# Kernel optimization log

Measured on AMD Instinct MI355X. Metric: run time of the kernel, lower is better.

## Reference

```python
import jax, jax.numpy as jnp
import numpy as np

PAD = 7                 # init padding
T = 2 * PAD + 1         # T_side_dense = 15 shifts per axis
LAMDA = 1.0             # init lamda
EPS = 1e-16             # hardcoded epsilon in the torch loss body


def _joint_hist(x_out, x_tf_out):
    # Equivalent of F.conv2d(x_out.permute(1,0,2,3), weight=x_tf_out.permute(1,0,2,3), padding=PAD)
    # expressed as T*T shifted matmuls (correlation / cost-volume form).
    bn, k, h, w = x_out.shape
    A = jnp.transpose(x_out, (1, 0, 2, 3))      # (k, bn, h, w)  conv "input"
    B = jnp.transpose(x_tf_out, (1, 0, 2, 3))   # (k, bn, h, w)  conv "weight"
    A_pad = jnp.pad(A, ((0, 0), (0, 0), (PAD, PAD), (PAD, PAD)))

    def step(carry, s):
        dy, dx = s // T, s % T
        sl = jax.lax.dynamic_slice(A_pad, (0, 0, dy, dx), (k, bn, h, w))
        # p[n, o] at this shift = sum_{c,y,x} A_pad[n,c,y+dy,x+dx] * B[o,c,y,x]
        return carry, jnp.einsum('nchw,ochw->no', sl, B)

    _, p = jax.lax.scan(step, None, jnp.arange(T * T))
    # (T*T, k, k) -> (T, T, k, k); matches torch p_i_j.permute(2, 3, 0, 1)
    return p.reshape(T, T, k, k)


def reference(x_out, x_tf_out):
    p = _joint_hist(x_out, x_tf_out)
    # shift to positive; min is detached in torch -> stop_gradient
    p = p - jax.lax.stop_gradient(p.min()) + EPS
    # normalize per shift over the (k, k) joint
    p = p / p.sum(axis=(2, 3), keepdims=True)
    # symmetrize
    p = (p + jnp.swapaxes(p, 2, 3)) / 2.0
    p_i = p.sum(axis=2, keepdims=True)   # (T, T, 1, k) marginal (broadcasts like repeat)
    p_j = p.sum(axis=3, keepdims=True)   # (T, T, k, 1) marginal
    loss = (-p * (jnp.log(p + EPS)
                  - LAMDA * jnp.log(p_i + EPS)
                  - LAMDA * jnp.log(p_j + EPS))).sum() / (T * T)
    return loss


def setup_inputs() -> dict:
    key = jax.random.key(0)
    k1, k2 = jax.random.split(key)
    bn, k, h, w = 16, 10, 224, 224
    # simplex over axis=1 is asserted by the torch module -> use softmax
    x_out = jax.nn.softmax(jax.random.normal(k1, (bn, k, h, w), dtype=jnp.float32), axis=1)
    x_tf_out = jax.nn.softmax(jax.random.normal(k2, (bn, k, h, w), dtype=jnp.float32), axis=1)
    return {"x_out": x_out, "x_tf_out": x_tf_out}
```

## Files before the change

### kernel.cpp

```cpp
#include <hip/hip_runtime.h>
#include <stdint.h>
#include <math.h>


#define PADV 7
#define TS 15
#define KCLS 10
#define HH 224
#define WW 224
#define MD 160
#define NCELL (MD*MD)
#define NBLK 256
#define TY 14
#define BSTRIDE 232
#define BSTRIDE_L 236
#define BPH 240
#define PLANEE 2408
#define ABUFE (8*PLANEE)
#define NRED 400
#define LEPS 1e-16

typedef __attribute__((ext_vector_type(4))) float f32x4;
typedef __attribute__((ext_vector_type(8))) short bf16x8;

__device__ __forceinline__ unsigned short f2bf(float f) {
  union { float f; uint32_t u; } v; v.f = f;
  return (unsigned short)((v.u + 0x7FFFu + ((v.u >> 16) & 1u)) >> 16);
}

__device__ __forceinline__ uint32_t pack2bf(float a, float b) {
  return (uint32_t)f2bf(a) | ((uint32_t)f2bf(b) << 16);
}

__device__ __forceinline__ void glds16(const unsigned short* g, unsigned short* l) {
  __builtin_amdgcn_global_load_lds(
      (const __attribute__((address_space(1))) unsigned int*)g,
      (__attribute__((address_space(3))) unsigned int*)l, 16, 0, 0);
}

__device__ __forceinline__ void plane_write(const f32x4 f[4], unsigned short* awr) {
  uint32_t w[8];
#pragma unroll
  for (int k = 0; k < 8; ++k)
    w[k] = pack2bf(f[k >> 1][(k & 1) * 2], f[k >> 1][(k & 1) * 2 + 1]);
#pragma unroll
  for (int c = 0; c < 8; ++c) {
    union { uint32_t u[4]; uint4 v; } o;
    if (c & 1) {
#pragma unroll
      for (int j = 0; j < 4; ++j) o.u[j] = w[j + (c + 1) / 2];
    } else {
#pragma unroll
      for (int j = 0; j < 4; ++j)
        o.u[j] = __builtin_amdgcn_alignbit(w[j + 1 + c / 2], w[j + c / 2], 16);
    }
    *(uint4*)(awr + c * PLANEE) = o.v;
  }
}

__global__ __launch_bounds__(256)
void prep_b(const float* __restrict__ xt, unsigned short* __restrict__ bp) {
  const int idx   = blockIdx.x * 256 + threadIdx.x;
  const int rowid = idx / 29;
  const int chunk = idx - rowid * 29;
  const int x0    = chunk * 8;
  const int yy    = rowid % BPH;
  const int cls   = rowid / BPH;
  const int row   = yy - PADV;
  union { unsigned short h[8]; uint4 v; } out;
  if (row >= 0 && row < HH && chunk < 28) {
    const float4* src = (const float4*)(xt + ((size_t)cls * HH + row) * WW + x0);
    const float4 f0 = src[0], f1 = src[1];
    out.h[0] = f2bf(f0.x); out.h[1] = f2bf(f0.y);
    out.h[2] = f2bf(f0.z); out.h[3] = f2bf(f0.w);
    out.h[4] = f2bf(f1.x); out.h[5] = f2bf(f1.y);
    out.h[6] = f2bf(f1.z); out.h[7] = f2bf(f1.w);
  } else {
    out.v = make_uint4(0u, 0u, 0u, 0u);
  }
  *(uint4*)(bp + (size_t)rowid * BSTRIDE + x0) = out.v;
}

#define MFMA_BF16 __builtin_amdgcn_mfma_f32_16x16x32_bf16

__global__ __launch_bounds__(640, 1)
void corr_gemm(const float* __restrict__ xo, const unsigned short* __restrict__ bpad,
               float* __restrict__ partials) {
  __shared__ __align__(16) unsigned short ldsA8[2 * ABUFE];
  __shared__ __align__(16) unsigned short ldsB[KCLS * 16 * BSTRIDE_L];

  const int tid  = threadIdx.x;
  const int bid0 = blockIdx.x;
  const int bid  = (bid0 & 7) * 32 + (bid0 >> 3);
  const int b    = bid >> 4;
  const int y0   = (bid & 15) * TY;

  const int lane = tid & 63;
  const int wv   = tid >> 6;
  const int wm   = wv >> 1;
  const int wn   = wv & 1;
  const int quad = lane >> 4;
  const int l15  = lane & 15;

  f32x4 acc[2][5];
#pragma unroll
  for (int i = 0; i < 2; ++i)
#pragma unroll
    for (int j = 0; j < 5; ++j) acc[i][j] = (f32x4){0.f, 0.f, 0.f, 0.f};

  const float* Ab = xo + (size_t)b * KCLS * HH * WW;
  const unsigned short* Bb = bpad + (size_t)b * KCLS * BPH * BSTRIDE;

  const bool aw  = tid < 300;
  const int an   = aw ? tid / 30 : 0;
  const int atp  = aw ? tid - (tid / 30) * 30 : 0;
  const int axb  = atp * 8 - 8;
  bool gv[4];
#pragma unroll
  for (int g = 0; g < 4; ++g)
    gv[g] = aw && (axb + 4 * g >= 0) && (axb + 4 * g + 4 <= WW);
  unsigned short* const awr0 = ldsA8 + an * 240 + atp * 8;

  for (int pr = wv; pr < 15 * KCLS; pr += 10) {
    const int r15  = pr / KCLS;
    const int o    = pr - r15 * KCLS;
    const int yy   = y0 + r15;
    const int slot = (y0 - PADV + r15) & 15;
    if (lane < 29)
      glds16(Bb + ((size_t)o * BPH + yy) * BSTRIDE + lane * 8,
             ldsB + (o * 16 + slot) * BSTRIDE_L);
  }

  f32x4 f[4];
  {
    const float* src = Ab + ((size_t)an * HH + y0) * WW + axb;
#pragma unroll
    for (int g = 0; g < 4; ++g) {
      f[g] = (f32x4){0.f, 0.f, 0.f, 0.f};
      if (gv[g]) f[g] = *(const f32x4*)(src + 4 * g);
    }
  }
  if (aw) plane_write(f, awr0);
  __syncthreads();

  int cur = 0;
  for (int s = 0; s < TY; ++s) {
    const int y = y0 + s;
    const bool more = (s + 1 < TY);

    if (more) {
      const int yy   = y + 8 + PADV;
      const int slot = (y + 8) & 15;
      if (lane < 29)
        glds16(Bb + ((size_t)wv * BPH + yy) * BSTRIDE + lane * 8,
               ldsB + (wv * 16 + slot) * BSTRIDE_L);
      const float* src = Ab + ((size_t)an * HH + (y + 1)) * WW + axb;
#pragma unroll
      for (int g = 0; g < 4; ++g) {
        f[g] = (f32x4){0.f, 0.f, 0.f, 0.f};
        if (gv[g]) f[g] = *(const f32x4*)(src + 4 * g);
      }
    }

    const unsigned short* paB = ldsA8 + cur * ABUFE + (l15 & 7) * PLANEE + (l15 & 8);
    const int slotB = (y + PADV - l15) & 15;

#pragma unroll 2
    for (int xc = 0; xc < 7; ++xc) {
      const int x0 = xc * 32;
      bf16x8 afrag[2], bfrag[5];
#pragma unroll
      for (int mi = 0; mi < 2; ++mi)
        afrag[mi] = *(const bf16x8*)(paB + (wm * 2 + mi) * 240 + x0 + quad * 8);
#pragma unroll
      for (int ni = 0; ni < 5; ++ni) {
        const int to = wn * 5 + ni;
        bfrag[ni] = *(const bf16x8*)(ldsB + (to * 16 + slotB) * BSTRIDE_L + x0 + quad * 8);
      }
#pragma unroll
      for (int mi = 0; mi < 2; ++mi)
#pragma unroll
        for (int ni = 0; ni < 5; ++ni)
          acc[mi][ni] = MFMA_BF16(afrag[mi], bfrag[ni], acc[mi][ni], 0, 0, 0);
    }

    if (more) {
      if (aw) plane_write(f, awr0 + (cur ^ 1) * ABUFE);
      __syncthreads();
      cur ^= 1;
    }
  }

  float* outp = partials + (size_t)bid * NCELL;
#pragma unroll
  for (int mi = 0; mi < 2; ++mi)
#pragma unroll
    for (int ni = 0; ni < 5; ++ni) {
      const int mrow = (wm * 2 + mi) * 16 + quad * 4;
      const int ncol = (wn * 5 + ni) * 16 + l15;
#pragma unroll
      for (int r = 0; r < 4; ++r)
        outp[(size_t)(mrow + r) * MD + ncol] = acc[mi][ni][r];
    }
}

__global__ __launch_bounds__(256)
void reduce_all(const float* __restrict__ partials, float* __restrict__ Cout,
                float* __restrict__ mins, float* __restrict__ dout) {
  const int tid = threadIdx.x;
  const int cl  = tid & 63;
  const int g   = tid >> 6;
  const int c   = blockIdx.x * 64 + cl;
  if (blockIdx.x == 0 && tid == 0) dout[0] = 0.f;

  const float* base = partials + (size_t)g * 64 * NCELL + c;
  double s0 = 0.0, s1 = 0.0, s2 = 0.0, s3 = 0.0;
  for (int p = 0; p < 64; p += 4) {
    s0 += (double)base[(size_t)(p + 0) * NCELL];
    s1 += (double)base[(size_t)(p + 1) * NCELL];
    s2 += (double)base[(size_t)(p + 2) * NCELL];
    s3 += (double)base[(size_t)(p + 3) * NCELL];
  }
  __shared__ double redd[256];
  redd[tid] = (s0 + s1) + (s2 + s3);
  __syncthreads();

  __shared__ float redm[64];
  if (tid < 64) {
    const double tot = redd[tid] + redd[tid + 64] + redd[tid + 128] + redd[tid + 192];
    const float sf = (float)tot;
    Cout[c] = sf;
    const int m  = c / MD;
    const int nn = c - m * MD;
    const bool valid = ((m & 15) < TS) && ((nn & 15) < TS);
    redm[tid] = valid ? sf : 3.4e38f;
  }
  __syncthreads();
  for (int st = 32; st > 0; st >>= 1) {
    if (tid < st) redm[tid] = fminf(redm[tid], redm[tid + st]);
    __syncthreads();
  }
  if (tid == 0) mins[blockIdx.x] = redm[0];
}

__global__ __launch_bounds__(128)
void loss_kernel(const float* __restrict__ Cmat, const float* __restrict__ mins,
                 float* __restrict__ dout) {
  const int s   = blockIdx.x;
  const int dy  = s / TS;
  const int dx  = s - dy * TS;
  const int tid = threadIdx.x;
  __shared__ float fm[128];
  __shared__ double q[100];
  __shared__ double sym[100];
  __shared__ double pi[10], pj[10];
  __shared__ double red[128];

  {
    float v = 3.4e38f;
    for (int i = tid; i < NRED; i += 128) v = fminf(v, mins[i]);
    fm[tid] = v;
  }
  __syncthreads();
  for (int st = 64; st > 0; st >>= 1) {
    if (tid < st) fm[tid] = fminf(fm[tid], fm[tid + st]);
    __syncthreads();
  }
  const double minv = (double)fm[0];
  __syncthreads();

  if (tid < 100) {
    const int n = tid / 10, o = tid - (tid / 10) * 10;
    const double v = (double)Cmat[(size_t)(n * 16 + dx) * MD + (o * 16 + dy)];
    q[tid] = v - minv + LEPS;
  }
  __syncthreads();
  red[tid] = (tid < 100) ? q[tid] : 0.0;
  __syncthreads();
  for (int st = 64; st > 0; st >>= 1) {
    if (tid < st) red[tid] += red[tid + st];
    __syncthreads();
  }
  const double Z = red[0];
  __syncthreads();
  if (tid < 100) {
    const int n = tid / 10, o = tid - (tid / 10) * 10;
    sym[tid] = (q[n * 10 + o] + q[o * 10 + n]) * 0.5 / Z;
  }
  __syncthreads();
  if (tid < 10) {
    double a = 0.0, bsum = 0.0;
    for (int n2 = 0; n2 < 10; ++n2) {
      a    += sym[n2 * 10 + tid];
      bsum += sym[tid * 10 + n2];
    }
    pi[tid] = a;
    pj[tid] = bsum;
  }
  __syncthreads();
  double term = 0.0;
  if (tid < 100) {
    const int n = tid / 10, o = tid - (tid / 10) * 10;
    const double sp = sym[tid];
    term = -sp * (log(sp + LEPS) - log(pi[o] + LEPS) - log(pj[n] + LEPS));
  }
  red[tid] = term;
  __syncthreads();
  for (int st = 64; st > 0; st >>= 1) {
    if (tid < st) red[tid] += red[tid + st];
    __syncthreads();
  }
  if (tid == 0) atomicAdd(dout, (float)(red[0] / (double)(TS * TS)));
}

extern "C" void kernel_launch(void* const* d_in, const int* in_sizes, int n_in,
                              void* d_out, int out_size, void* d_ws, size_t ws_size,
                              hipStream_t stream) {
  const float* xo = (const float*)d_in[0];
  const float* xt = (const float*)d_in[1];
  float* ws       = (float*)d_ws;

  float* partials = ws;
  float* Cmat     = partials + (size_t)NBLK * NCELL;
  float* mins     = Cmat + NCELL;
  unsigned short* bpad = (unsigned short*)(mins + 512);
  float* out      = (float*)d_out;

  hipLaunchKernelGGL(prep_b,      dim3(4350), dim3(256), 0, stream, xt, bpad);
  hipLaunchKernelGGL(corr_gemm,   dim3(NBLK), dim3(640), 0, stream, xo, bpad, partials);
  hipLaunchKernelGGL(reduce_all,  dim3(NRED), dim3(256), 0, stream, partials, Cmat, mins, out);
  hipLaunchKernelGGL(loss_kernel, dim3(225),  dim3(128), 0, stream, Cmat, mins, out);
}
```

Before: 146.5 us.

## Fuse prep, GEMM, reduction and loss into one cooperative kernel with grid syncs

Merges the four kernels (bf16 padding prep, correlation GEMM, partial reduction, loss) into one cooperative kernel of 256 blocks of 640 threads. Grid-wide syncs separate the phases and shared memory is reused across them. This removes three kernel launch gaps and tail effects. In exchange, prep and reduction now run on only 256 blocks, grid syncs have their own cost, and cooperative launch requires all blocks to be resident at once.

```diff
diff --git a/kernel.cpp b/kernel.cpp
--- a/kernel.cpp
+++ b/kernel.cpp
@@ -1,6 +1,9 @@
 #include <hip/hip_runtime.h>
+#include <hip/hip_cooperative_groups.h>
 #include <stdint.h>
 #include <math.h>
+
+namespace cg = cooperative_groups;
 
 
 #define PADV 7
@@ -17,7 +20,10 @@
 #define BPH 240
 #define PLANEE 2408
 #define ABUFE (8*PLANEE)
-#define NRED 400
+#define LDSA_BYTES (2*ABUFE*2)
+#define LDSB_L_BYTES (KCLS*16*BSTRIDE_L*2)
+#define SMEM_BYTES (LDSA_BYTES + LDSB_L_BYTES)
+#define NPREP (38400*29)
 #define LEPS 1e-16
 
 typedef __attribute__((ext_vector_type(4))) float f32x4;
@@ -58,259 +64,269 @@
   }
 }
 
-__global__ __launch_bounds__(256)
-void prep_b(const float* __restrict__ xt, unsigned short* __restrict__ bp) {
-  const int idx   = blockIdx.x * 256 + threadIdx.x;
-  const int rowid = idx / 29;
-  const int chunk = idx - rowid * 29;
-  const int x0    = chunk * 8;
-  const int yy    = rowid % BPH;
-  const int cls   = rowid / BPH;
-  const int row   = yy - PADV;
-  union { unsigned short h[8]; uint4 v; } out;
-  if (row >= 0 && row < HH && chunk < 28) {
-    const float4* src = (const float4*)(xt + ((size_t)cls * HH + row) * WW + x0);
-    const float4 f0 = src[0], f1 = src[1];
-    out.h[0] = f2bf(f0.x); out.h[1] = f2bf(f0.y);
-    out.h[2] = f2bf(f0.z); out.h[3] = f2bf(f0.w);
-    out.h[4] = f2bf(f1.x); out.h[5] = f2bf(f1.y);
-    out.h[6] = f2bf(f1.z); out.h[7] = f2bf(f1.w);
-  } else {
-    out.v = make_uint4(0u, 0u, 0u, 0u);
-  }
-  *(uint4*)(bp + (size_t)rowid * BSTRIDE + x0) = out.v;
-}
-
 #define MFMA_BF16 __builtin_amdgcn_mfma_f32_16x16x32_bf16
 
 __global__ __launch_bounds__(640, 1)
-void corr_gemm(const float* __restrict__ xo, const unsigned short* __restrict__ bpad,
-               float* __restrict__ partials) {
-  __shared__ __align__(16) unsigned short ldsA8[2 * ABUFE];
-  __shared__ __align__(16) unsigned short ldsB[KCLS * 16 * BSTRIDE_L];
-
-  const int tid  = threadIdx.x;
-  const int bid0 = blockIdx.x;
-  const int bid  = (bid0 & 7) * 32 + (bid0 >> 3);
-  const int b    = bid >> 4;
-  const int y0   = (bid & 15) * TY;
-
-  const int lane = tid & 63;
-  const int wv   = tid >> 6;
-  const int wm   = wv >> 1;
-  const int wn   = wv & 1;
-  const int quad = lane >> 4;
-  const int l15  = lane & 15;
-
-  f32x4 acc[2][5];
-#pragma unroll
-  for (int i = 0; i < 2; ++i)
-#pragma unroll
-    for (int j = 0; j < 5; ++j) acc[i][j] = (f32x4){0.f, 0.f, 0.f, 0.f};
-
-  const float* Ab = xo + (size_t)b * KCLS * HH * WW;
-  const unsigned short* Bb = bpad + (size_t)b * KCLS * BPH * BSTRIDE;
-
-  const bool aw  = tid < 300;
-  const int an   = aw ? tid / 30 : 0;
-  const int atp  = aw ? tid - (tid / 30) * 30 : 0;
-  const int axb  = atp * 8 - 8;
-  bool gv[4];
-#pragma unroll
-  for (int g = 0; g < 4; ++g)
-    gv[g] = aw && (axb + 4 * g >= 0) && (axb + 4 * g + 4 <= WW);
-  unsigned short* const awr0 = ldsA8 + an * 240 + atp * 8;
-
-  for (int pr = wv; pr < 15 * KCLS; pr += 10) {
-    const int r15  = pr / KCLS;
-    const int o    = pr - r15 * KCLS;
-    const int yy   = y0 + r15;
-    const int slot = (y0 - PADV + r15) & 15;
-    if (lane < 29)
-      glds16(Bb + ((size_t)o * BPH + yy) * BSTRIDE + lane * 8,
-             ldsB + (o * 16 + slot) * BSTRIDE_L);
-  }
-
-  f32x4 f[4];
+void fused_all(const float* __restrict__ xo, const float* __restrict__ xt,
+               unsigned short* __restrict__ bpad, float* __restrict__ partials,
+               float* __restrict__ Cmat, float* __restrict__ mins,
+               float* __restrict__ dout) {
+  __shared__ __align__(16) unsigned char smem[SMEM_BYTES];
+  cg::grid_group grid = cg::this_grid();
+  const int tid = threadIdx.x;
+
+  for (int idx = blockIdx.x * 640 + tid; idx < NPREP; idx += NBLK * 640) {
+    const int rowid = idx / 29;
+    const int chunk = idx - rowid * 29;
+    const int x0    = chunk * 8;
+    const int yy    = rowid % BPH;
+    const int cls   = rowid / BPH;
+    const int row   = yy - PADV;
+    union { unsigned short h[8]; uint4 v; } out;
+    if (row >= 0 && row < HH && chunk < 28) {
+      const float4* src = (const float4*)(xt + ((size_t)cls * HH + row) * WW + x0);
+      const float4 f0 = src[0], f1 = src[1];
+      out.h[0] = f2bf(f0.x); out.h[1] = f2bf(f0.y);
+      out.h[2] = f2bf(f0.z); out.h[3] = f2bf(f0.w);
+      out.h[4] = f2bf(f1.x); out.h[5] = f2bf(f1.y);
+      out.h[6] = f2bf(f1.z); out.h[7] = f2bf(f1.w);
+    } else {
+      out.v = make_uint4(0u, 0u, 0u, 0u);
+    }
+    *(uint4*)(bpad + (size_t)rowid * BSTRIDE + x0) = out.v;
+  }
+  grid.sync();
+
   {
-    const float* src = Ab + ((size_t)an * HH + y0) * WW + axb;
-#pragma unroll
-    for (int g = 0; g < 4; ++g) {
-      f[g] = (f32x4){0.f, 0.f, 0.f, 0.f};
-      if (gv[g]) f[g] = *(const f32x4*)(src + 4 * g);
-    }
-  }
-  if (aw) plane_write(f, awr0);
-  __syncthreads();
-
-  int cur = 0;
-  for (int s = 0; s < TY; ++s) {
-    const int y = y0 + s;
-    const bool more = (s + 1 < TY);
-
-    if (more) {
-      const int yy   = y + 8 + PADV;
-      const int slot = (y + 8) & 15;
+    unsigned short* const ldsA8 = (unsigned short*)smem;
+    unsigned short* const ldsB  = (unsigned short*)(smem + LDSA_BYTES);
+
+    const int bid0 = blockIdx.x;
+    const int bid  = (bid0 & 7) * 32 + (bid0 >> 3);
+    const int b    = bid >> 4;
+    const int y0   = (bid & 15) * TY;
+
+    const int lane = tid & 63;
+    const int wv   = tid >> 6;
+    const int wm   = wv >> 1;
+    const int wn   = wv & 1;
+    const int quad = lane >> 4;
+    const int l15  = lane & 15;
+
+    f32x4 acc[2][5];
+#pragma unroll
+    for (int i = 0; i < 2; ++i)
+#pragma unroll
+      for (int j = 0; j < 5; ++j) acc[i][j] = (f32x4){0.f, 0.f, 0.f, 0.f};
+
+    const float* Ab = xo + (size_t)b * KCLS * HH * WW;
+    const unsigned short* Bb = bpad + (size_t)b * KCLS * BPH * BSTRIDE;
+
+    const bool aw  = tid < 300;
+    const int an   = aw ? tid / 30 : 0;
+    const int atp  = aw ? tid - (tid / 30) * 30 : 0;
+    const int axb  = atp * 8 - 8;
+    bool gv[4];
+#pragma unroll
+    for (int g = 0; g < 4; ++g)
+      gv[g] = aw && (axb + 4 * g >= 0) && (axb + 4 * g + 4 <= WW);
+    unsigned short* const awr0 = ldsA8 + an * 240 + atp * 8;
+
+    for (int pr = wv; pr < 15 * KCLS; pr += 10) {
+      const int r15  = pr / KCLS;
+      const int o    = pr - r15 * KCLS;
+      const int yy   = y0 + r15;
+      const int slot = (y0 - PADV + r15) & 15;
       if (lane < 29)
-        glds16(Bb + ((size_t)wv * BPH + yy) * BSTRIDE + lane * 8,
-               ldsB + (wv * 16 + slot) * BSTRIDE_L);
-      const float* src = Ab + ((size_t)an * HH + (y + 1)) * WW + axb;
+        glds16(Bb + ((size_t)o * BPH + yy) * BSTRIDE + lane * 8,
+               ldsB + (o * 16 + slot) * BSTRIDE_L);
+    }
+
+    f32x4 f[4];
+    {
+      const float* src = Ab + ((size_t)an * HH + y0) * WW + axb;
 #pragma unroll
       for (int g = 0; g < 4; ++g) {
         f[g] = (f32x4){0.f, 0.f, 0.f, 0.f};
         if (gv[g]) f[g] = *(const f32x4*)(src + 4 * g);
       }
     }
-
-    const unsigned short* paB = ldsA8 + cur * ABUFE + (l15 & 7) * PLANEE + (l15 & 8);
-    const int slotB = (y + PADV - l15) & 15;
+    if (aw) plane_write(f, awr0);
+    __syncthreads();
+
+    int cur = 0;
+    for (int s = 0; s < TY; ++s) {
+      const int y = y0 + s;
+      const bool more = (s + 1 < TY);
+
+      if (more) {
+        const int yy   = y + 8 + PADV;
+        const int slot = (y + 8) & 15;
+        if (lane < 29)
+          glds16(Bb + ((size_t)wv * BPH + yy) * BSTRIDE + lane * 8,
+                 ldsB + (wv * 16 + slot) * BSTRIDE_L);
+        const float* src = Ab + ((size_t)an * HH + (y + 1)) * WW + axb;
+#pragma unroll
+        for (int g = 0; g < 4; ++g) {
+          f[g] = (f32x4){0.f, 0.f, 0.f, 0.f};
+          if (gv[g]) f[g] = *(const f32x4*)(src + 4 * g);
+        }
+      }
+
+      const unsigned short* paB = ldsA8 + cur * ABUFE + (l15 & 7) * PLANEE + (l15 & 8);
+      const int slotB = (y + PADV - l15) & 15;
 
 #pragma unroll 2
-    for (int xc = 0; xc < 7; ++xc) {
-      const int x0 = xc * 32;
-      bf16x8 afrag[2], bfrag[5];
-#pragma unroll
-      for (int mi = 0; mi < 2; ++mi)
-        afrag[mi] = *(const bf16x8*)(paB + (wm * 2 + mi) * 240 + x0 + quad * 8);
+      for (int xc = 0; xc < 7; ++xc) {
+        const int x0 = xc * 32;
+        bf16x8 afrag[2], bfrag[5];
+#pragma unroll
+        for (int mi = 0; mi < 2; ++mi)
+          afrag[mi] = *(const bf16x8*)(paB + (wm * 2 + mi) * 240 + x0 + quad * 8);
+#pragma unroll
+        for (int ni = 0; ni < 5; ++ni) {
+          const int to = wn * 5 + ni;
+          bfrag[ni] = *(const bf16x8*)(ldsB + (to * 16 + slotB) * BSTRIDE_L + x0 + quad * 8);
+        }
+#pragma unroll
+        for (int mi = 0; mi < 2; ++mi)
+#pragma unroll
+          for (int ni = 0; ni < 5; ++ni)
+            acc[mi][ni] = MFMA_BF16(afrag[mi], bfrag[ni], acc[mi][ni], 0, 0, 0);
+      }
+
+      if (more) {
+        if (aw) plane_write(f, awr0 + (cur ^ 1) * ABUFE);
+        __syncthreads();
+        cur ^= 1;
+      }
+    }
+
+    float* outp = partials + (size_t)bid * NCELL;
+#pragma unroll
+    for (int mi = 0; mi < 2; ++mi)
 #pragma unroll
       for (int ni = 0; ni < 5; ++ni) {
-        const int to = wn * 5 + ni;
-        bfrag[ni] = *(const bf16x8*)(ldsB + (to * 16 + slotB) * BSTRIDE_L + x0 + quad * 8);
-      }
-#pragma unroll
-      for (int mi = 0; mi < 2; ++mi)
-#pragma unroll
-        for (int ni = 0; ni < 5; ++ni)
-          acc[mi][ni] = MFMA_BF16(afrag[mi], bfrag[ni], acc[mi][ni], 0, 0, 0);
-    }
-
-    if (more) {
-      if (aw) plane_write(f, awr0 + (cur ^ 1) * ABUFE);
+        const int mrow = (wm * 2 + mi) * 16 + quad * 4;
+        const int ncol = (wn * 5 + ni) * 16 + l15;
+#pragma unroll
+        for (int r = 0; r < 4; ++r)
+          outp[(size_t)(mrow + r) * MD + ncol] = acc[mi][ni][r];
+      }
+  }
+  grid.sync();
+
+  {
+    double* redd = (double*)smem;
+    float*  redm = (float*)(smem + 4096);
+    if (blockIdx.x == 0 && tid == 0) dout[0] = 0.f;
+    const int c0 = blockIdx.x * 100;
+    if (tid < 400) {
+      const int g  = tid / 100;
+      const int cl = tid - g * 100;
+      const float* base = partials + (size_t)g * 64 * NCELL + c0 + cl;
+      double s0 = 0.0, s1 = 0.0, s2 = 0.0, s3 = 0.0;
+      for (int p = 0; p < 64; p += 4) {
+        s0 += (double)base[(size_t)(p + 0) * NCELL];
+        s1 += (double)base[(size_t)(p + 1) * NCELL];
+        s2 += (double)base[(size_t)(p + 2) * NCELL];
+        s3 += (double)base[(size_t)(p + 3) * NCELL];
+      }
+      redd[tid] = (s0 + s1) + (s2 + s3);
+    }
+    __syncthreads();
+    if (tid < 128) {
+      float mv = 3.4e38f;
+      if (tid < 100) {
+        const double tot = redd[tid] + redd[tid + 100] + redd[tid + 200] + redd[tid + 300];
+        const float sf = (float)tot;
+        const int c = c0 + tid;
+        Cmat[c] = sf;
+        const int m  = c / MD;
+        const int nn = c - m * MD;
+        if (((m & 15) < TS) && ((nn & 15) < TS)) mv = sf;
+      }
+      redm[tid] = mv;
+    }
+    __syncthreads();
+    for (int st = 64; st > 0; st >>= 1) {
+      if (tid < st) redm[tid] = fminf(redm[tid], redm[tid + st]);
       __syncthreads();
-      cur ^= 1;
-    }
-  }
-
-  float* outp = partials + (size_t)bid * NCELL;
-#pragma unroll
-  for (int mi = 0; mi < 2; ++mi)
-#pragma unroll
-    for (int ni = 0; ni < 5; ++ni) {
-      const int mrow = (wm * 2 + mi) * 16 + quad * 4;
-      const int ncol = (wn * 5 + ni) * 16 + l15;
-#pragma unroll
-      for (int r = 0; r < 4; ++r)
-        outp[(size_t)(mrow + r) * MD + ncol] = acc[mi][ni][r];
-    }
-}
-
-__global__ __launch_bounds__(256)
-void reduce_all(const float* __restrict__ partials, float* __restrict__ Cout,
-                float* __restrict__ mins, float* __restrict__ dout) {
-  const int tid = threadIdx.x;
-  const int cl  = tid & 63;
-  const int g   = tid >> 6;
-  const int c   = blockIdx.x * 64 + cl;
-  if (blockIdx.x == 0 && tid == 0) dout[0] = 0.f;
-
-  const float* base = partials + (size_t)g * 64 * NCELL + c;
-  double s0 = 0.0, s1 = 0.0, s2 = 0.0, s3 = 0.0;
-  for (int p = 0; p < 64; p += 4) {
-    s0 += (double)base[(size_t)(p + 0) * NCELL];
-    s1 += (double)base[(size_t)(p + 1) * NCELL];
-    s2 += (double)base[(size_t)(p + 2) * NCELL];
-    s3 += (double)base[(size_t)(p + 3) * NCELL];
-  }
-  __shared__ double redd[256];
-  redd[tid] = (s0 + s1) + (s2 + s3);
-  __syncthreads();
-
-  __shared__ float redm[64];
-  if (tid < 64) {
-    const double tot = redd[tid] + redd[tid + 64] + redd[tid + 128] + redd[tid + 192];
-    const float sf = (float)tot;
-    Cout[c] = sf;
-    const int m  = c / MD;
-    const int nn = c - m * MD;
-    const bool valid = ((m & 15) < TS) && ((nn & 15) < TS);
-    redm[tid] = valid ? sf : 3.4e38f;
-  }
-  __syncthreads();
-  for (int st = 32; st > 0; st >>= 1) {
-    if (tid < st) redm[tid] = fminf(redm[tid], redm[tid + st]);
-    __syncthreads();
-  }
-  if (tid == 0) mins[blockIdx.x] = redm[0];
-}
-
-__global__ __launch_bounds__(128)
-void loss_kernel(const float* __restrict__ Cmat, const float* __restrict__ mins,
-                 float* __restrict__ dout) {
-  const int s   = blockIdx.x;
-  const int dy  = s / TS;
-  const int dx  = s - dy * TS;
-  const int tid = threadIdx.x;
-  __shared__ float fm[128];
-  __shared__ double q[100];
-  __shared__ double sym[100];
-  __shared__ double pi[10], pj[10];
-  __shared__ double red[128];
-
-  {
-    float v = 3.4e38f;
-    for (int i = tid; i < NRED; i += 128) v = fminf(v, mins[i]);
-    fm[tid] = v;
-  }
-  __syncthreads();
-  for (int st = 64; st > 0; st >>= 1) {
-    if (tid < st) fm[tid] = fminf(fm[tid], fm[tid + st]);
-    __syncthreads();
-  }
-  const double minv = (double)fm[0];
-  __syncthreads();
-
-  if (tid < 100) {
-    const int n = tid / 10, o = tid - (tid / 10) * 10;
-    const double v = (double)Cmat[(size_t)(n * 16 + dx) * MD + (o * 16 + dy)];
-    q[tid] = v - minv + LEPS;
-  }
-  __syncthreads();
-  red[tid] = (tid < 100) ? q[tid] : 0.0;
-  __syncthreads();
-  for (int st = 64; st > 0; st >>= 1) {
-    if (tid < st) red[tid] += red[tid + st];
-    __syncthreads();
-  }
-  const double Z = red[0];
-  __syncthreads();
-  if (tid < 100) {
-    const int n = tid / 10, o = tid - (tid / 10) * 10;
-    sym[tid] = (q[n * 10 + o] + q[o * 10 + n]) * 0.5 / Z;
-  }
-  __syncthreads();
-  if (tid < 10) {
-    double a = 0.0, bsum = 0.0;
-    for (int n2 = 0; n2 < 10; ++n2) {
-      a    += sym[n2 * 10 + tid];
-      bsum += sym[tid * 10 + n2];
-    }
-    pi[tid] = a;
-    pj[tid] = bsum;
-  }
-  __syncthreads();
-  double term = 0.0;
-  if (tid < 100) {
-    const int n = tid / 10, o = tid - (tid / 10) * 10;
-    const double sp = sym[tid];
-    term = -sp * (log(sp + LEPS) - log(pi[o] + LEPS) - log(pj[n] + LEPS));
-  }
-  red[tid] = term;
-  __syncthreads();
-  for (int st = 64; st > 0; st >>= 1) {
-    if (tid < st) red[tid] += red[tid + st];
-    __syncthreads();
-  }
-  if (tid == 0) atomicAdd(dout, (float)(red[0] / (double)(TS * TS)));
+    }
+    if (tid == 0) mins[blockIdx.x] = redm[0];
+  }
+  grid.sync();
+
+  if (blockIdx.x < TS * TS) {
+    float*  fm  = (float*)smem;
+    double* q   = (double*)(smem + 512);
+    double* sym = (double*)(smem + 1536);
+    double* pi  = (double*)(smem + 2560);
+    double* pj  = (double*)(smem + 2688);
+    double* red = (double*)(smem + 2816);
+
+    const int s  = blockIdx.x;
+    const int dy = s / TS;
+    const int dx = s - dy * TS;
+
+    if (tid < 128) {
+      float v = 3.4e38f;
+      for (int i = tid; i < NBLK; i += 128) v = fminf(v, mins[i]);
+      fm[tid] = v;
+    }
+    __syncthreads();
+    for (int st = 64; st > 0; st >>= 1) {
+      if (tid < st) fm[tid] = fminf(fm[tid], fm[tid + st]);
+      __syncthreads();
+    }
+    const double minv = (double)fm[0];
+    __syncthreads();
+
+    if (tid < 100) {
+      const int n = tid / 10, o = tid - (tid / 10) * 10;
+      const double v = (double)Cmat[(size_t)(n * 16 + dx) * MD + (o * 16 + dy)];
+      q[tid] = v - minv + LEPS;
+    }
+    __syncthreads();
+    if (tid < 128) red[tid] = (tid < 100) ? q[tid] : 0.0;
+    __syncthreads();
+    for (int st = 64; st > 0; st >>= 1) {
+      if (tid < st) red[tid] += red[tid + st];
+      __syncthreads();
+    }
+    const double Z = red[0];
+    __syncthreads();
+    if (tid < 100) {
+      const int n = tid / 10, o = tid - (tid / 10) * 10;
+      sym[tid] = (q[n * 10 + o] + q[o * 10 + n]) * 0.5 / Z;
+    }
+    __syncthreads();
+    if (tid < 10) {
+      double a = 0.0, bsum = 0.0;
+      for (int n2 = 0; n2 < 10; ++n2) {
+        a    += sym[n2 * 10 + tid];
+        bsum += sym[tid * 10 + n2];
+      }
+      pi[tid] = a;
+      pj[tid] = bsum;
+    }
+    __syncthreads();
+    if (tid < 128) {
+      double term = 0.0;
+      if (tid < 100) {
+        const int n = tid / 10, o = tid - (tid / 10) * 10;
+        const double sp = sym[tid];
+        term = -sp * (log(sp + LEPS) - log(pi[o] + LEPS) - log(pj[n] + LEPS));
+      }
+      red[tid] = term;
+    }
+    __syncthreads();
+    for (int st = 64; st > 0; st >>= 1) {
+      if (tid < st) red[tid] += red[tid + st];
+      __syncthreads();
+    }
+    if (tid == 0) atomicAdd(dout, (float)(red[0] / (double)(TS * TS)));
+  }
 }
 
 extern "C" void kernel_launch(void* const* d_in, const int* in_sizes, int n_in,
@@ -326,8 +342,8 @@
   unsigned short* bpad = (unsigned short*)(mins + 512);
   float* out      = (float*)d_out;
 
-  hipLaunchKernelGGL(prep_b,      dim3(4350), dim3(256), 0, stream, xt, bpad);
-  hipLaunchKernelGGL(corr_gemm,   dim3(NBLK), dim3(640), 0, stream, xo, bpad, partials);
-  hipLaunchKernelGGL(reduce_all,  dim3(NRED), dim3(256), 0, stream, partials, Cmat, mins, out);
-  hipLaunchKernelGGL(loss_kernel, dim3(225),  dim3(128), 0, stream, Cmat, mins, out);
-}
+  void* args[] = {(void*)&xo, (void*)&xt, (void*)&bpad, (void*)&partials,
+                  (void*)&Cmat, (void*)&mins, (void*)&out};
+  hipLaunchCooperativeKernel((const void*)fused_all, dim3(NBLK), dim3(640),
+                             args, 0, stream);
+}
```

After: 351.2 us. 140% more time.

## Switch correlation GEMM to 32x32 MFMA with split-K across wave groups

Applied to the files above, without the earlier changes.

Replaces the 16x16x32 bf16 MFMA tiling, where each wave covered a 2x5 grid of 16x16 tiles over the full width, with 32x32x16 MFMA. Each wave now owns one 32-row strip against five 32-column tiles. The ten waves are split into two K-groups that each take half of the x range. The two halves are reduced through an LDS scratch area that aliases the A/B buffers before being written to global memory. The goal is fewer LDS fragment loads per FLOP and a higher MFMA share, at the cost of an extra barrier-synchronised LDS reduction in the epilogue and larger accumulator register pressure.

```diff
diff --git a/kernel.cpp b/kernel.cpp
--- a/kernel.cpp
+++ b/kernel.cpp
@@ -17,10 +17,14 @@
 #define BPH 240
 #define PLANEE 2408
 #define ABUFE (8*PLANEE)
+#define LDSA_BYTES (2*ABUFE*2)
+#define LDSB_L_BYTES (KCLS*16*BSTRIDE_L*2)
+#define SMEM_BYTES (LDSA_BYTES + LDSB_L_BYTES)
 #define NRED 400
 #define LEPS 1e-16
 
 typedef __attribute__((ext_vector_type(4))) float f32x4;
+typedef __attribute__((ext_vector_type(16))) float f32x16;
 typedef __attribute__((ext_vector_type(8))) short bf16x8;
 
 __device__ __forceinline__ unsigned short f2bf(float f) {
@@ -81,13 +85,15 @@
   *(uint4*)(bp + (size_t)rowid * BSTRIDE + x0) = out.v;
 }
 
-#define MFMA_BF16 __builtin_amdgcn_mfma_f32_16x16x32_bf16
+#define MFMA32 __builtin_amdgcn_mfma_f32_32x32x16_bf16
 
 __global__ __launch_bounds__(640, 1)
 void corr_gemm(const float* __restrict__ xo, const unsigned short* __restrict__ bpad,
                float* __restrict__ partials) {
-  __shared__ __align__(16) unsigned short ldsA8[2 * ABUFE];
-  __shared__ __align__(16) unsigned short ldsB[KCLS * 16 * BSTRIDE_L];
+  __shared__ __align__(16) unsigned char smem[SMEM_BYTES];
+  unsigned short* const ldsA8 = (unsigned short*)smem;
+  unsigned short* const ldsB  = (unsigned short*)(smem + LDSA_BYTES);
+  float* const scratch        = (float*)smem;
 
   const int tid  = threadIdx.x;
   const int bid0 = blockIdx.x;
@@ -97,16 +103,15 @@
 
   const int lane = tid & 63;
   const int wv   = tid >> 6;
-  const int wm   = wv >> 1;
-  const int wn   = wv & 1;
-  const int quad = lane >> 4;
+  const int kg   = (wv >= 5);
+  const int w5   = kg ? wv - 5 : wv;
   const int l15  = lane & 15;
-
-  f32x4 acc[2][5];
-#pragma unroll
-  for (int i = 0; i < 2; ++i)
-#pragma unroll
-    for (int j = 0; j < 5; ++j) acc[i][j] = (f32x4){0.f, 0.f, 0.f, 0.f};
+  const int oh   = (lane >> 4) & 1;
+  const int kh   = lane >> 5;
+
+  f32x16 a0, a1, a2, a3, a4;
+#pragma unroll
+  for (int j = 0; j < 16; ++j) { a0[j]=0.f; a1[j]=0.f; a2[j]=0.f; a3[j]=0.f; a4[j]=0.f; }
 
   const float* Ab = xo + (size_t)b * KCLS * HH * WW;
   const unsigned short* Bb = bpad + (size_t)b * KCLS * BPH * BSTRIDE;
@@ -143,6 +148,7 @@
   if (aw) plane_write(f, awr0);
   __syncthreads();
 
+  const int ksB = kg ? 7 : 0;
   int cur = 0;
   for (int s = 0; s < TY; ++s) {
     const int y = y0 + s;
@@ -162,26 +168,25 @@
       }
     }
 
-    const unsigned short* paB = ldsA8 + cur * ABUFE + (l15 & 7) * PLANEE + (l15 & 8);
+    const unsigned short* paA = ldsA8 + cur * ABUFE + (l15 & 7) * PLANEE +
+                                (l15 & 8) + (2 * w5 + oh) * 240 + kh * 8;
     const int slotB = (y + PADV - l15) & 15;
-
-#pragma unroll 2
-    for (int xc = 0; xc < 7; ++xc) {
-      const int x0 = xc * 32;
-      bf16x8 afrag[2], bfrag[5];
-#pragma unroll
-      for (int mi = 0; mi < 2; ++mi)
-        afrag[mi] = *(const bf16x8*)(paB + (wm * 2 + mi) * 240 + x0 + quad * 8);
-#pragma unroll
-      for (int ni = 0; ni < 5; ++ni) {
-        const int to = wn * 5 + ni;
-        bfrag[ni] = *(const bf16x8*)(ldsB + (to * 16 + slotB) * BSTRIDE_L + x0 + quad * 8);
-      }
-#pragma unroll
-      for (int mi = 0; mi < 2; ++mi)
-#pragma unroll
-        for (int ni = 0; ni < 5; ++ni)
-          acc[mi][ni] = MFMA_BF16(afrag[mi], bfrag[ni], acc[mi][ni], 0, 0, 0);
+    const unsigned short* pB = ldsB + (oh * 16 + slotB) * BSTRIDE_L + kh * 8;
+
+#pragma unroll 1
+    for (int ks = ksB; ks < ksB + 7; ++ks) {
+      const int xq = ks * 16;
+      const bf16x8 af = *(const bf16x8*)(paA + xq);
+      const bf16x8 bf0 = *(const bf16x8*)(pB + 0 * 32 * BSTRIDE_L + xq);
+      const bf16x8 bf1 = *(const bf16x8*)(pB + 1 * 32 * BSTRIDE_L + xq);
+      const bf16x8 bf2 = *(const bf16x8*)(pB + 2 * 32 * BSTRIDE_L + xq);
+      const bf16x8 bf3 = *(const bf16x8*)(pB + 3 * 32 * BSTRIDE_L + xq);
+      const bf16x8 bf4 = *(const bf16x8*)(pB + 4 * 32 * BSTRIDE_L + xq);
+      a0 = MFMA32(af, bf0, a0, 0, 0, 0);
+      a1 = MFMA32(af, bf1, a1, 0, 0, 0);
+      a2 = MFMA32(af, bf2, a2, 0, 0, 0);
+      a3 = MFMA32(af, bf3, a3, 0, 0, 0);
+      a4 = MFMA32(af, bf4, a4, 0, 0, 0);
     }
 
     if (more) {
@@ -191,17 +196,36 @@
     }
   }
 
-  float* outp = partials + (size_t)bid * NCELL;
-#pragma unroll
-  for (int mi = 0; mi < 2; ++mi)
-#pragma unroll
-    for (int ni = 0; ni < 5; ++ni) {
-      const int mrow = (wm * 2 + mi) * 16 + quad * 4;
-      const int ncol = (wn * 5 + ni) * 16 + l15;
-#pragma unroll
-      for (int r = 0; r < 4; ++r)
-        outp[(size_t)(mrow + r) * MD + ncol] = acc[mi][ni][r];
-    }
+  __syncthreads();
+  if (kg == 1) {
+#define EPI_ST(T, ARR)                                                        \
+    _Pragma("unroll")                                                         \
+    for (int p = 0; p < 4; ++p) {                                             \
+      f32x4 v;                                                                \
+      _Pragma("unroll")                                                       \
+      for (int j = 0; j < 4; ++j) v[j] = ARR[4 * p + j];                      \
+      *(f32x4*)(scratch + ((w5 * 5 + (T)) * 4 + p) * 256 + lane * 4) = v;     \
+    }
+    EPI_ST(0, a0) EPI_ST(1, a1) EPI_ST(2, a2) EPI_ST(3, a3) EPI_ST(4, a4)
+#undef EPI_ST
+  }
+  __syncthreads();
+  if (kg == 0) {
+    float* outp = partials + (size_t)bid * NCELL;
+    const int c32 = lane & 31;
+#define EPI_WR(T, ARR)                                                        \
+    _Pragma("unroll")                                                         \
+    for (int p = 0; p < 4; ++p) {                                             \
+      f32x4 v = *(const f32x4*)(scratch +                                     \
+                 ((w5 * 5 + (T)) * 4 + p) * 256 + lane * 4);                  \
+      _Pragma("unroll")                                                       \
+      for (int j = 0; j < 4; ++j)                                             \
+        outp[(size_t)(w5 * 32 + j + 8 * p + 4 * kh) * MD + (T) * 32 + c32] =  \
+            v[j] + ARR[4 * p + j];                                            \
+    }
+    EPI_WR(0, a0) EPI_WR(1, a1) EPI_WR(2, a2) EPI_WR(3, a3) EPI_WR(4, a4)
+#undef EPI_WR
+  }
 }
 
 __global__ __launch_bounds__(256)
```

After: 257.8 us. 76.0% more time.
